# Kernel optimization log

Hardware: AMD Instinct MI355X
Metric: run time of the kernel (lower is better)

## Reference

```python
import jax, jax.numpy as jnp
import numpy as np
from jax import lax

B, L, D = 2, 4096, 2048
H = 16
DK = D // H  # head qk dim == head v dim == 128
CONV = 4
EPS = 1e-5


def _causal_depthwise_conv(x, w):
    # x: [b, l, c], w: [c, K]; torch-style cross-correlation with left padding K-1
    K = w.shape[1]
    xp = jnp.pad(x, ((0, 0), (K - 1, 0), (0, 0)))
    Lx = x.shape[1]
    y = jnp.zeros_like(x)
    for i in range(K):
        y = y + xp[:, i:i + Lx, :] * w[:, i]
    return y


def _l2norm(x):
    return x / jnp.sqrt(jnp.sum(x * x, axis=-1, keepdims=True) + 1e-12)


def _delta_rule(q, k, v, beta):
    # q,k: [b,h,l,dk]; v: [b,h,l,dv]; beta: [b,h,l]
    b, h, l, dk = q.shape
    dv = v.shape[-1]
    qs = jnp.moveaxis(q, 2, 0)
    ks = jnp.moveaxis(k, 2, 0)
    vs = jnp.moveaxis(v, 2, 0)
    bs = jnp.moveaxis(beta, 2, 0)

    def step(S, inp):
        qt, kt, vt, bt = inp  # [b,h,dk],[b,h,dk],[b,h,dv],[b,h]
        kS = jnp.einsum('bhk,bhkv->bhv', kt, S)
        u = bt[..., None] * (vt - kS)
        S = S + kt[..., None] * u[:, :, None, :]
        o = jnp.einsum('bhk,bhkv->bhv', qt, S)
        return S, o

    S0 = jnp.zeros((b, h, dk, dv), dtype=q.dtype)
    _, os = lax.scan(step, S0, (qs, ks, vs, bs))
    return jnp.moveaxis(os, 0, 2)  # [b,h,l,dv]


def setup_inputs() -> dict:
    key = jax.random.key(0)
    ks = jax.random.split(key, 8)
    s = 0.02
    return {
        'hidden_states': jax.random.normal(ks[0], (B, L, D), jnp.float32),
        'w_cattn': jax.random.normal(ks[1], (D, 3 * D), jnp.float32) * s,
        'wq_conv': jax.random.normal(ks[2], (D, CONV), jnp.float32) * 0.3,
        'wk_conv': jax.random.normal(ks[3], (D, CONV), jnp.float32) * 0.3,
        'wv_conv': jax.random.normal(ks[4], (D, CONV), jnp.float32) * 0.3,
        'w_beta': jax.random.normal(ks[5], (D, H), jnp.float32) * s,
        'o_norm_w': jnp.ones((DK,), jnp.float32),
        'w_o': jax.random.normal(ks[6], (D, D), jnp.float32) * s,
    }


def reference(hidden_states, w_cattn, wq_conv, wk_conv, wv_conv, w_beta, o_norm_w, w_o):
    qkv = hidden_states @ w_cattn  # [b,l,3D]
    q, k, v = jnp.split(qkv, 3, axis=-1)
    # short conv + SiLU activation (qk_activation='silu', v conv always SiLU)
    q = jax.nn.silu(_causal_depthwise_conv(q, wq_conv))
    k = jax.nn.silu(_causal_depthwise_conv(k, wk_conv))
    v = jax.nn.silu(_causal_depthwise_conv(v, wv_conv))
    # b l (h d) -> b h l d
    def to_heads(x):
        return jnp.transpose(x.reshape(B, L, H, -1), (0, 2, 1, 3))
    q, k, v = to_heads(q), to_heads(k), to_heads(v)
    # qk_norm = 'l2'
    q = _l2norm(q)
    k = _l2norm(k)
    beta = jax.nn.sigmoid(hidden_states @ w_beta)  # [b,l,h]
    beta = jnp.transpose(beta, (0, 2, 1))  # [b,h,l]
    o = _delta_rule(q, k, v, beta)  # [b,h,l,dv]
    o = jnp.transpose(o, (0, 2, 1, 3))  # [b,l,h,dv]
    # RMSNorm over head_v_dim
    o = o * lax.rsqrt(jnp.mean(o * o, axis=-1, keepdims=True) + EPS) * o_norm_w
    o = o.reshape(B, L, D)
    return o @ w_o
```

## Files before the change

kernel.cpp:

```cpp
#include <hip/hip_runtime.h>
#include <stdint.h>

#define B_   2
#define L_   4096
#define D_   2048
#define H_   16
#define DK_  128
#define ND3  6144
#define BL_  8192

typedef __bf16 bf16x8 __attribute__((ext_vector_type(8)));
typedef float  f32x4  __attribute__((ext_vector_type(4)));

__device__ __forceinline__ float bf2f(ushort u){ return __uint_as_float(((unsigned)u)<<16); }
__device__ __forceinline__ ushort f2bf(float f){
  unsigned u = __float_as_uint(f);
  unsigned r = u + 0x7FFFu + ((u>>16)&1u);
  return (ushort)(r>>16);
}
__device__ __forceinline__ f32x4 mfma16(bf16x8 a, bf16x8 b, f32x4 c){
  return __builtin_amdgcn_mfma_f32_16x16x32_bf16(a, b, c, 0, 0, 0);
}

#define BAR_LGKM() do{ __builtin_amdgcn_sched_barrier(0); \
  asm volatile("s_waitcnt lgkmcnt(0)" ::: "memory"); \
  __builtin_amdgcn_s_barrier(); \
  __builtin_amdgcn_sched_barrier(0);}while(0)
#define BAR_VMALL() do{ __builtin_amdgcn_sched_barrier(0); \
  asm volatile("s_waitcnt vmcnt(0) lgkmcnt(0)" ::: "memory"); \
  __builtin_amdgcn_s_barrier(); \
  __builtin_amdgcn_sched_barrier(0);}while(0)

__global__ __launch_bounds__(256) void k_cast(const float* __restrict__ x, ushort* __restrict__ y, int n4){
  int i = blockIdx.x*blockDim.x + threadIdx.x;
  int stride = gridDim.x*blockDim.x;
  for (; i < n4; i += stride){
    float4 v = ((const float4*)x)[i];
    ushort4 o; o.x=f2bf(v.x); o.y=f2bf(v.y); o.z=f2bf(v.z); o.w=f2bf(v.w);
    ((ushort4*)y)[i] = o;
  }
}

__global__ __launch_bounds__(256) void k_transpose_cast(const float* __restrict__ in, ushort* __restrict__ out,
                                                        int R, int C){
  __shared__ float tile[32][33];
  int c0 = blockIdx.x*32, r0 = blockIdx.y*32;
  int tx = threadIdx.x, ty = threadIdx.y;
  #pragma unroll
  for (int i=0;i<32;i+=8) tile[ty+i][tx] = in[(size_t)(r0+ty+i)*C + (c0+tx)];
  __syncthreads();
  #pragma unroll
  for (int i=0;i<32;i+=8) out[(size_t)(c0+ty+i)*R + (r0+tx)] = f2bf(tile[tx][ty+i]);
}

template<int OUT_BF16>
__global__ __launch_bounds__(512, 1) void k_gemm8(const ushort* __restrict__ A, const ushort* __restrict__ Bt,
                                                  void* __restrict__ Cv, int M, int N, int K){
  __shared__ ushort LDSB[65536];
  char* lds = (char*)LDSB;
  const int tid = threadIdx.x, lane = tid & 63, w = tid >> 6;
  const int wm = w >> 2, wn = w & 3;
  int nwg = gridDim.x*gridDim.y;
  int id  = blockIdx.y*gridDim.x + blockIdx.x;
  int sw  = ((nwg & 7) == 0) ? ((id & 7)*(nwg >> 3) + (id >> 3)) : id;
  const int bx = sw % gridDim.x, by = sw / gridDim.x;
  const int m0 = by*256, n0 = bx*256;
  const int NT = K >> 6;
  const size_t rowb = (size_t)K*2;
  const char* gA = (const char*)A  + (size_t)m0*rowb;
  const char* gB = (const char*)Bt + (size_t)n0*rowb;

  f32x4 acc[8][4];
  #pragma unroll
  for (int i=0;i<8;i++)
    #pragma unroll
    for (int j=0;j<4;j++) acc[i][j] = (f32x4){0.f,0.f,0.f,0.f};

  auto stage = [&](int d2, int which, int T){
    const int isB = which >> 1, h = which & 1;
    const char* g = isB ? gB : gA;
    char* halfbase = lds + d2*65536 + isB*32768 + h*16384;
    #pragma unroll
    for (int uu=0; uu<2; ++uu){
      int u = tid + uu*512;
      int band = u >> 7, kk = (u >> 6) & 1, lr = u & 15, lk = (u >> 4) & 3;
      const char* src = g + (size_t)(h*128 + band*16 + lr)*rowb + (size_t)T*128 + kk*64 + lk*16;
      __builtin_amdgcn_global_load_lds(
        (const __attribute__((address_space(1))) void*)src,
        (__attribute__((address_space(3))) void*)(halfbase + u*16), 16, 0, 0);
    }
  };

  stage(0, 0, 0); stage(0, 1, 0); stage(0, 2, 0); stage(0, 3, 0);
  {
    int t1 = (1 < NT) ? 1 : 0;
    stage(1, 0, t1); stage(1, 3, t1);
  }
  asm volatile("s_waitcnt vmcnt(4)" ::: "memory");
  __builtin_amdgcn_s_barrier();

  for (int t = 0; t < NT; ++t){
    const int d = t & 1;
    const char* bufb = lds + d*65536;
    const int tn1 = (t+1 < NT) ? t+1 : NT-1;
    const int tn2 = (t+2 < NT) ? t+2 : NT-1;

    bf16x8 afr[4][2];
    bf16x8 b0r[2][2], b1r[2][2];

    #pragma unroll
    for (int il=0; il<4; ++il)
      #pragma unroll
      for (int kk=0; kk<2; ++kk)
        afr[il][kk] = *(const bf16x8*)(bufb + ((wm*4+il)*2+kk)*1024 + lane*16);
    #pragma unroll
    for (int jl=0; jl<2; ++jl)
      #pragma unroll
      for (int kk=0; kk<2; ++kk)
        b0r[jl][kk] = *(const bf16x8*)(bufb + 32768 + ((wn*2+jl)*2+kk)*1024 + lane*16);
    stage(d^1, 1, tn1);
    __builtin_amdgcn_s_barrier();
    __builtin_amdgcn_s_setprio(1);
    #pragma unroll
    for (int kk=0; kk<2; ++kk)
      #pragma unroll
      for (int il=0; il<4; ++il)
        #pragma unroll
        for (int jl=0; jl<2; ++jl)
          acc[il][jl] = mfma16(afr[il][kk], b0r[jl][kk], acc[il][jl]);
    __builtin_amdgcn_s_setprio(0);
    __builtin_amdgcn_s_barrier();

    #pragma unroll
    for (int jl=0; jl<2; ++jl)
      #pragma unroll
      for (int kk=0; kk<2; ++kk)
        b1r[jl][kk] = *(const bf16x8*)(bufb + 32768 + 16384 + ((wn*2+jl)*2+kk)*1024 + lane*16);
    stage(d^1, 2, tn1);
    __builtin_amdgcn_s_barrier();
    __builtin_amdgcn_s_setprio(1);
    #pragma unroll
    for (int kk=0; kk<2; ++kk)
      #pragma unroll
      for (int il=0; il<4; ++il)
        #pragma unroll
        for (int jl=0; jl<2; ++jl)
          acc[il][2+jl] = mfma16(afr[il][kk], b1r[jl][kk], acc[il][2+jl]);
    __builtin_amdgcn_s_setprio(0);
    __builtin_amdgcn_s_barrier();

    #pragma unroll
    for (int il=0; il<4; ++il)
      #pragma unroll
      for (int kk=0; kk<2; ++kk)
        afr[il][kk] = *(const bf16x8*)(bufb + 16384 + ((wm*4+il)*2+kk)*1024 + lane*16);
    stage(d, 0, tn2);
    __builtin_amdgcn_s_barrier();
    __builtin_amdgcn_s_setprio(1);
    #pragma unroll
    for (int kk=0; kk<2; ++kk)
      #pragma unroll
      for (int il=0; il<4; ++il)
        #pragma unroll
        for (int jl=0; jl<2; ++jl)
          acc[4+il][2+jl] = mfma16(afr[il][kk], b1r[jl][kk], acc[4+il][2+jl]);
    __builtin_amdgcn_s_setprio(0);
    __builtin_amdgcn_s_barrier();

    stage(d, 3, tn2);
    __builtin_amdgcn_s_barrier();
    __builtin_amdgcn_s_setprio(1);
    #pragma unroll
    for (int kk=0; kk<2; ++kk)
      #pragma unroll
      for (int il=0; il<4; ++il)
        #pragma unroll
        for (int jl=0; jl<2; ++jl)
          acc[4+il][jl] = mfma16(afr[il][kk], b0r[jl][kk], acc[4+il][jl]);
    __builtin_amdgcn_s_setprio(0);
    asm volatile("s_waitcnt vmcnt(4)" ::: "memory");
    __builtin_amdgcn_s_barrier();
  }
  asm volatile("s_waitcnt vmcnt(0) lgkmcnt(0)" ::: "memory");

  #pragma unroll
  for (int fi=0; fi<8; ++fi){
    int row0 = m0 + (fi>>2)*128 + wm*64 + (fi&3)*16 + (lane>>4)*4;
    #pragma unroll
    for (int fj=0; fj<4; ++fj){
      int col = n0 + (fj>>1)*128 + wn*32 + (fj&1)*16 + (lane&15);
      #pragma unroll
      for (int r=0; r<4; ++r){
        float v = acc[fi][fj][r];
        if (OUT_BF16) ((ushort*)Cv)[(size_t)(row0+r)*N + col] = f2bf(v);
        else          ((float*) Cv)[(size_t)(row0+r)*N + col] = v;
      }
    }
  }
}

__global__ __launch_bounds__(256) void k_wbt(const float* __restrict__ wb, ushort* __restrict__ wbT){
  int d = blockIdx.x*256 + threadIdx.x;
  #pragma unroll
  for (int h=0;h<16;h++) wbT[(size_t)h*2048 + d] = f2bf(wb[(size_t)d*16 + h]);
}

__global__ __launch_bounds__(64) void k_beta2(const ushort* __restrict__ A16, const ushort* __restrict__ wbT,
                                              float* __restrict__ beta){
  const int rt = blockIdx.x;
  const int lane = threadIdx.x;
  const int lr = lane & 15, lk8 = (lane>>4)*8;
  const int r0 = rt*16;
  f32x4 acc0 = (f32x4){0.f,0.f,0.f,0.f};
  f32x4 acc1 = (f32x4){0.f,0.f,0.f,0.f};
  for (int k0=0; k0<2048; k0+=64){
    bf16x8 a0 = *(const bf16x8*)&A16[(size_t)(r0+lr)*2048 + k0 + lk8];
    bf16x8 b0 = *(const bf16x8*)&wbT[(size_t)lr*2048 + k0 + lk8];
    bf16x8 a1 = *(const bf16x8*)&A16[(size_t)(r0+lr)*2048 + k0 + 32 + lk8];
    bf16x8 b1 = *(const bf16x8*)&wbT[(size_t)lr*2048 + k0 + 32 + lk8];
    acc0 = mfma16(a0, b0, acc0);
    acc1 = mfma16(a1, b1, acc1);
  }
  const int h = lane & 15;
  const int rbase = r0 + (lane>>4)*4;
  #pragma unroll
  for (int r=0;r<4;r++){
    int row = rbase + r;
    int b = row >> 12, l = row & 4095;
    float sg = 1.f/(1.f + __expf(-(acc0[r] + acc1[r])));
    beta[((size_t)(b*H_ + h))*L_ + l] = sg;
  }
}

__global__ __launch_bounds__(256) void k_conv2(const ushort* __restrict__ qkv,
      const float* __restrict__ wq, const float* __restrict__ wk, const float* __restrict__ wv,
      ushort* __restrict__ QH, ushort* __restrict__ KH, ushort* __restrict__ VH){
  const int seg = blockIdx.x, part = blockIdx.y, b = blockIdx.z;
  const int t = threadIdx.x;
  const int ch = t*8;
  const int h = t >> 4, d0 = (t & 15)*8;
  const float* wc = (part==0) ? wq : (part==1) ? wk : wv;
  ushort* outs = ((part==0) ? QH : (part==1) ? KH : VH)
                 + ((size_t)(b*H_ + h)*L_)*DK_ + d0;
  const ushort* inp = qkv + ((size_t)b*L_)*ND3 + part*D_ + ch;

  float wgt[4][8];
  #pragma unroll
  for (int j=0;j<8;j++){
    float4 w4 = *(const float4*)&wc[(ch + j)*4];
    wgt[0][j]=w4.x; wgt[1][j]=w4.y; wgt[2][j]=w4.z; wgt[3][j]=w4.w;
  }

  const int l0 = seg*32;
  float x0[8], x1[8], x2[8];
  {
    float* dsts[3] = {x0, x1, x2};
    #pragma unroll
    for (int i=0;i<3;i++){
      int l = l0 - 3 + i;
      float* d = dsts[i];
      if (l >= 0){
        const ushort* p = inp + (size_t)l*ND3;
        ushort4 a = *(const ushort4*)p, c = *(const ushort4*)(p+4);
        d[0]=bf2f(a.x); d[1]=bf2f(a.y); d[2]=bf2f(a.z); d[3]=bf2f(a.w);
        d[4]=bf2f(c.x); d[5]=bf2f(c.y); d[6]=bf2f(c.z); d[7]=bf2f(c.w);
      } else {
        #pragma unroll
        for (int j=0;j<8;j++) d[j] = 0.f;
      }
    }
  }

  for (int i=0;i<32;i++){
    const int l = l0 + i;
    float cur[8];
    {
      const ushort* p = inp + (size_t)l*ND3;
      ushort4 a = *(const ushort4*)p, c = *(const ushort4*)(p+4);
      cur[0]=bf2f(a.x); cur[1]=bf2f(a.y); cur[2]=bf2f(a.z); cur[3]=bf2f(a.w);
      cur[4]=bf2f(c.x); cur[5]=bf2f(c.y); cur[6]=bf2f(c.z); cur[7]=bf2f(c.w);
    }
    float y[8]; float ss = 0.f;
    #pragma unroll
    for (int j=0;j<8;j++){
      float yy = x0[j]*wgt[0][j] + x1[j]*wgt[1][j] + x2[j]*wgt[2][j] + cur[j]*wgt[3][j];
      yy = yy / (1.f + __expf(-yy));
      y[j] = yy; ss += yy*yy;
    }
    if (part < 2){
      #pragma unroll
      for (int m=1;m<16;m<<=1) ss += __shfl_xor(ss, m, 64);
      float sc = rsqrtf(ss + 1e-12f);
      #pragma unroll
      for (int j=0;j<8;j++) y[j] *= sc;
    }
    ushort4 o0, o1;
    o0.x=f2bf(y[0]); o0.y=f2bf(y[1]); o0.z=f2bf(y[2]); o0.w=f2bf(y[3]);
    o1.x=f2bf(y[4]); o1.y=f2bf(y[5]); o1.z=f2bf(y[6]); o1.w=f2bf(y[7]);
    ushort* op = outs + (size_t)l*DK_;
    *(ushort4*)op = o0; *(ushort4*)(op+4) = o1;
    #pragma unroll
    for (int j=0;j<8;j++){ x0[j]=x1[j]; x1[j]=x2[j]; x2[j]=cur[j]; }
  }
}

__global__ __launch_bounds__(64) void k_prep(const ushort* __restrict__ QH, const ushort* __restrict__ KH,
      const float* __restrict__ BETA, ushort* __restrict__ TB, ushort* __restrict__ MM,
      ushort* __restrict__ KT){
  const int bid = blockIdx.x, bh = bid>>6, c = bid&63;
  const int lane = threadIdx.x;
  __shared__ ushort Ks[64][136];
  __shared__ __align__(16) char QA[17408];
  __shared__ float bs[64];
  ushort (*Qs)[136] = (ushort (*)[136])QA;
  float  (*As)[64]  = (float  (*)[64])QA;

  const ushort* kg = KH + ((size_t)bh*L_ + c*64)*DK_;
  const ushort* qg = QH + ((size_t)bh*L_ + c*64)*DK_;
  {
    const uint4* ks4 = (const uint4*)(kg + (size_t)lane*DK_);
    const uint4* qs4 = (const uint4*)(qg + (size_t)lane*DK_);
    uint4* kd = (uint4*)&Ks[lane][0];
    uint4* qd = (uint4*)&Qs[lane][0];
    #pragma unroll
    for (int i=0;i<16;i++){ kd[i] = ks4[i]; qd[i] = qs4[i]; }
    bs[lane] = BETA[(size_t)bh*L_ + c*64 + lane];
  }
  __syncthreads();
  const int lr = lane&15, lk = lane>>4;

  f32x4 gac[4][4];
  #pragma unroll
  for (int i=0;i<4;i++)
    #pragma unroll
    for (int j=0;j<4;j++) gac[i][j] = (f32x4){0.f,0.f,0.f,0.f};
  #pragma unroll
  for (int kk=0;kk<4;kk++){
    bf16x8 fr[4];
    #pragma unroll
    for (int i=0;i<4;i++) fr[i] = *(const bf16x8*)&Ks[i*16+lr][kk*32 + lk*8];
    #pragma unroll
    for (int mi=0;mi<4;mi++)
      #pragma unroll
      for (int ni=0;ni<4;ni++)
        gac[mi][ni] = mfma16(fr[mi], fr[ni], gac[mi][ni]);
  }
  {
    f32x4 mac[4][4];
    #pragma unroll
    for (int i=0;i<4;i++)
      #pragma unroll
      for (int j=0;j<4;j++) mac[i][j] = (f32x4){0.f,0.f,0.f,0.f};
    #pragma unroll
    for (int kk=0;kk<4;kk++){
      bf16x8 frq[4], frk[4];
      #pragma unroll
      for (int i=0;i<4;i++){
        frq[i] = *(const bf16x8*)&Qs[i*16+lr][kk*32 + lk*8];
        frk[i] = *(const bf16x8*)&Ks[i*16+lr][kk*32 + lk*8];
      }
      #pragma unroll
      for (int mi=0;mi<4;mi++)
        #pragma unroll
        for (int ni=0;ni<4;ni++)
          mac[mi][ni] = mfma16(frq[mi], frk[ni], mac[mi][ni]);
    }
    #pragma unroll
    for (int mi=0;mi<4;mi++)
      #pragma unroll
      for (int ni=0;ni<4;ni++)
        #pragma unroll
        for (int r=0;r<4;r++){
          int t = mi*16 + lk*4 + r, s = ni*16 + lr;
          float v = (s <= t) ? mac[mi][ni][r] : 0.f;
          MM[(size_t)bid*4096 + t*64 + s] = f2bf(v);
        }
  }
  __syncthreads();

  #pragma unroll
  for (int mi=0;mi<4;mi++)
    #pragma unroll
    for (int ni=0;ni<4;ni++)
      #pragma unroll
      for (int r=0;r<4;r++){
        int t = mi*16 + lk*4 + r, s = ni*16 + lr;
        As[t][s] = (s < t) ? (bs[t] * gac[mi][ni][r]) : 0.f;
      }
  __syncthreads();

  float rT[64];
  #pragma unroll
  for (int t=0;t<64;t++){
    float arow = As[t][lane];
    float a = (t==lane) ? 1.f : 0.f;
    #pragma unroll
    for (int s=0;s<t;s++){
      float cc = __int_as_float(__builtin_amdgcn_readlane(__float_as_int(arow), s));
      a -= cc * rT[s];
    }
    rT[t] = a;
  }
  {
    float bc = bs[lane];
    #pragma unroll
    for (int t=0;t<64;t++)
      TB[(size_t)bid*4096 + t*64 + lane] = f2bf(rT[t] * bc);
  }
  for (int d2=0; d2<64; d2++){
    unsigned uu = *(const unsigned*)&Ks[lane][2*d2];
    KT[(size_t)bid*8192 + (size_t)(2*d2)*64 + lane]   = (ushort)(uu & 0xffffu);
    KT[(size_t)bid*8192 + (size_t)(2*d2+1)*64 + lane] = (ushort)(uu >> 16);
  }
}

template<int LRB, int GRB, int NB, int XM>
__device__ __forceinline__ void stage_swz(const ushort* __restrict__ g, ushort* l,
                                          int colOff, int w, int lane){
  for (int idx = w; idx < NB/1024; idx += 4){
    int off = idx*1024 + lane*16;
    int row = off / LRB;
    int inner = off & (LRB-1);
    int src = row*GRB + colOff + (inner ^ ((row&XM)<<4));
    __builtin_amdgcn_global_load_lds(
      (const __attribute__((address_space(1))) void*)((const char*)g + src),
      (__attribute__((address_space(3))) void*)((char*)l + idx*1024), 16, 0, 0);
  }
}

__global__ __launch_bounds__(256) void k_chunkrec(const ushort* __restrict__ QH, const ushort* __restrict__ KH,
      const ushort* __restrict__ VH, const ushort* __restrict__ TB, const ushort* __restrict__ MM,
      const ushort* __restrict__ KT, ushort* __restrict__ OH){
  const int p = blockIdx.x;
  const int xg = p & 7, s = p >> 3;
  const int bh = xg + (s >> 3)*8;
  const int vo = s & 7;
  const int tid = threadIdx.x, lane = tid&63, w = tid>>6;
  const int lr = lane&15, lk = lane>>4;
  const int tw = w*16;
  const int dw = w*32;

  __shared__ ushort SM[71680];
  ushort* Stl = SM + 67584;
  ushort* Ztl = SM + 69632;
  ushort* Utl = SM + 70656;

  const ushort* kbase  = KH + ((size_t)bh*L_)*DK_;
  const ushort* qbase  = QH + ((size_t)bh*L_)*DK_;
  const ushort* vbase  = VH + ((size_t)bh*L_)*DK_;
  const ushort* tbase  = TB + ((size_t)bh*64)*4096;
  const ushort* mbase  = MM + ((size_t)bh*64)*4096;
  const ushort* ktbase = KT + ((size_t)bh*64)*8192;
  ushort* obase = OH + ((size_t)bh*L_)*DK_ + vo*16;

  auto stageall = [&](ushort* buf, int c){
    stage_swz<256,256,16384,7>(kbase  + (size_t)c*8192, buf,         0,     w, lane);
    stage_swz<256,256,16384,7>(qbase  + (size_t)c*8192, buf + 8192,  0,     w, lane);
    stage_swz<128,128,16384,7>(ktbase + (size_t)c*8192, buf + 16384, 0,     w, lane);
    stage_swz<128,128, 8192,7>(tbase  + (size_t)c*4096, buf + 24576, 0,     w, lane);
    stage_swz<128,128, 8192,7>(mbase  + (size_t)c*4096, buf + 28672, 0,     w, lane);
    stage_swz< 32,256, 2048,0>(vbase  + (size_t)c*8192, buf + 32768, vo*32, w, lane);
  };

  f32x4 Stf[2];
  Stf[0] = (f32x4){0.f,0.f,0.f,0.f};
  Stf[1] = (f32x4){0.f,0.f,0.f,0.f};

  stageall(SM, 0);
  BAR_VMALL();

  for (int c=0; c<64; ++c){
    ushort* buf  = SM + (c&1)*33792;
    ushort* nbuf = SM + ((c+1)&1)*33792;
    const ushort* Kc  = buf;
    const ushort* Qc  = buf + 8192;
    const ushort* Ktc = buf + 16384;
    const ushort* Tbc = buf + 24576;
    const ushort* Mc  = buf + 28672;
    const ushort* Vc  = buf + 32768;

    if (c+1 < 64) stageall(nbuf, c+1);

    #pragma unroll
    for (int nd=0;nd<2;nd++)
      #pragma unroll
      for (int r=0;r<4;r++){
        int j = lk*4 + r;
        int d = dw + nd*16 + lr;
        Stl[j*128 + (d ^ ((j&7)<<3))] = f2bf(Stf[nd][r]);
      }
    BAR_LGKM();

    f32x4 xac = (f32x4){0.f,0.f,0.f,0.f};
    #pragma unroll
    for (int kk=0;kk<4;kk++){
      int e = kk*32 + lk*8;
      int ta = tw + lr;
      bf16x8 ak  = *(const bf16x8*)&Kc[ta*128 + (e ^ ((ta&7)<<3))];
      bf16x8 bst = *(const bf16x8*)&Stl[lr*128 + (e ^ ((lr&7)<<3))];
      xac = mfma16(ak, bst, xac);
    }
    #pragma unroll
    for (int r=0;r<4;r++){
      int t = tw + lk*4 + r;
      int j = lr;
      float v = bf2f(Vc[t*16 + j]);
      Ztl[j*64 + (t ^ ((j&7)<<3))] = f2bf(v - xac[r]);
    }
    BAR_LGKM();

    f32x4 uac = (f32x4){0.f,0.f,0.f,0.f};
    #pragma unroll
    for (int kk=0;kk<2;kk++){
      int e = kk*32 + lk*8;
      int ta = tw + lr;
      bf16x8 at = *(const bf16x8*)&Tbc[ta*64 + (e ^ ((ta&7)<<3))];
      bf16x8 bz = *(const bf16x8*)&Ztl[lr*64 + (e ^ ((lr&7)<<3))];
      uac = mfma16(at, bz, uac);
    }
    #pragma unroll
    for (int r=0;r<4;r++){
      int t = tw + lk*4 + r;
      int j = lr;
      Utl[j*64 + (t ^ ((j&7)<<3))] = f2bf(uac[r]);
    }
    BAR_LGKM();

    f32x4 oac = (f32x4){0.f,0.f,0.f,0.f};
    #pragma unroll
    for (int kk=0;kk<4;kk++){
      int e = kk*32 + lk*8;
      int ta = tw + lr;
      bf16x8 aq  = *(const bf16x8*)&Qc[ta*128 + (e ^ ((ta&7)<<3))];
      bf16x8 bst = *(const bf16x8*)&Stl[lr*128 + (e ^ ((lr&7)<<3))];
      oac = mfma16(aq, bst, oac);
    }
    #pragma unroll
    for (int kk=0;kk<2;kk++){
      int e = kk*32 + lk*8;
      int ta = tw + lr;
      bf16x8 am = *(const bf16x8*)&Mc[ta*64 + (e ^ ((ta&7)<<3))];
      bf16x8 bu = *(const bf16x8*)&Utl[lr*64 + (e ^ ((lr&7)<<3))];
      oac = mfma16(am, bu, oac);
    }
    #pragma unroll
    for (int r=0;r<4;r++){
      int t = tw + lk*4 + r;
      int j = lr;
      obase[(size_t)(c*64 + t)*DK_ + j] = f2bf(oac[r]);
    }

    #pragma unroll
    for (int kk=0;kk<2;kk++){
      int e = kk*32 + lk*8;
      bf16x8 au = *(const bf16x8*)&Utl[lr*64 + (e ^ ((lr&7)<<3))];
      #pragma unroll
      for (int nd=0;nd<2;nd++){
        int d = dw + nd*16 + lr;
        bf16x8 bk = *(const bf16x8*)&Ktc[d*64 + (e ^ ((d&7)<<3))];
        Stf[nd] = mfma16(au, bk, Stf[nd]);
      }
    }
    BAR_VMALL();
  }
}

__global__ __launch_bounds__(256) void k_norm(const ushort* __restrict__ OH, const float* __restrict__ gw,
                                              ushort* __restrict__ O2){
  const int blk = blockIdx.x;
  const int b = blk >> 12, l = blk & 4095;
  const int t = threadIdx.x;
  const int h = t >> 4, d0 = (t & 15) * 8;
  const ushort* ip = OH + ((size_t)(b*H_ + h)*L_ + l)*DK_ + d0;
  ushort4 a = *(const ushort4*)ip, c = *(const ushort4*)(ip+4);
  float x[8];
  x[0]=bf2f(a.x); x[1]=bf2f(a.y); x[2]=bf2f(a.z); x[3]=bf2f(a.w);
  x[4]=bf2f(c.x); x[5]=bf2f(c.y); x[6]=bf2f(c.z); x[7]=bf2f(c.w);
  float ss = 0.f;
  #pragma unroll
  for (int j=0;j<8;j++) ss += x[j]*x[j];
  #pragma unroll
  for (int m=1;m<16;m<<=1) ss += __shfl_xor(ss, m, 64);
  float sc = rsqrtf(ss * (1.f/128.f) + 1e-5f);
  ushort* opp = O2 + (size_t)blk*D_ + h*DK_ + d0;
  ushort4 o0, o1;
  o0.x=f2bf(x[0]*sc*gw[d0+0]); o0.y=f2bf(x[1]*sc*gw[d0+1]);
  o0.z=f2bf(x[2]*sc*gw[d0+2]); o0.w=f2bf(x[3]*sc*gw[d0+3]);
  o1.x=f2bf(x[4]*sc*gw[d0+4]); o1.y=f2bf(x[5]*sc*gw[d0+5]);
  o1.z=f2bf(x[6]*sc*gw[d0+6]); o1.w=f2bf(x[7]*sc*gw[d0+7]);
  *(ushort4*)opp = o0; *(ushort4*)(opp+4) = o1;
}

extern "C" void kernel_launch(void* const* d_in, const int* in_sizes, int n_in,
                              void* d_out, int out_size, void* d_ws, size_t ws_size,
                              hipStream_t stream) {
  (void)in_sizes; (void)n_in; (void)out_size; (void)ws_size;
  const float* hidden  = (const float*)d_in[0];
  const float* w_cattn = (const float*)d_in[1];
  const float* wq_conv = (const float*)d_in[2];
  const float* wk_conv = (const float*)d_in[3];
  const float* wv_conv = (const float*)d_in[4];
  const float* w_beta  = (const float*)d_in[5];
  const float* o_nw    = (const float*)d_in[6];
  const float* w_o     = (const float*)d_in[7];
  float* out = (float*)d_out;

  char* W = (char*)d_ws;
  ushort* A16   = (ushort*)(W);
  ushort* WcatT = (ushort*)(W + 33554432u);
  ushort* WoT   = (ushort*)(W + 33554432u);
  float*  BETA  = (float*) (W + 41943040u);
  ushort* WBT   = (ushort*)(W + 42467328u);
  ushort* QKV   = (ushort*)(W + 58720256u);
  ushort* TB    = (ushort*)(W + 58720256u);
  ushort* MM    = (ushort*)(W + 75497472u);
  ushort* KT    = (ushort*)(W + 92274688u);
  ushort* O2    = (ushort*)(W + 125829120u);
  ushort* QH    = (ushort*)(W + 159383552u);
  ushort* KH    = (ushort*)(W + 192937984u);
  ushort* VH    = (ushort*)(W + 226492416u);
  ushort* OH = A16;

  k_cast<<<4096, 256, 0, stream>>>(hidden, A16, (BL_*D_)/4);
  k_transpose_cast<<<dim3(ND3/32, D_/32), dim3(32,8), 0, stream>>>(w_cattn, WcatT, D_, ND3);
  k_gemm8<1><<<dim3(ND3/256, BL_/256), 512, 0, stream>>>(A16, WcatT, QKV, BL_, ND3, D_);
  k_transpose_cast<<<dim3(D_/32, D_/32), dim3(32,8), 0, stream>>>(w_o, WoT, D_, D_);
  k_wbt<<<8, 256, 0, stream>>>(w_beta, WBT);
  k_beta2<<<512, 64, 0, stream>>>(A16, WBT, BETA);
  k_conv2<<<dim3(128, 3, 2), 256, 0, stream>>>(QKV, wq_conv, wk_conv, wv_conv, QH, KH, VH);
  k_prep<<<2048, 64, 0, stream>>>(QH, KH, BETA, TB, MM, KT);
  k_chunkrec<<<256, 256, 0, stream>>>(QH, KH, VH, TB, MM, KT, OH);
  k_norm<<<BL_, 256, 0, stream>>>(OH, o_nw, O2);
  k_gemm8<0><<<dim3(D_/256, BL_/256), 512, 0, stream>>>(O2, WoT, out, BL_, D_, D_);
}
```

Baseline: 574.5 us.

## Compute QK mask and K transpose inside chunk recurrence instead of prep

Moves the masked Q·K^T chunk matrix and the K transpose out of the prep kernel and into the chunk recurrence. There they are computed from the already-staged K and Q tiles in LDS. This removes writing and re-reading the MM and KT buffers through global memory and shrinks the per-chunk staging footprint. The cost is redundant recomputation across the eight value-slice blocks per head and more work inside the serial chunk loop.

```diff
diff --git a/kernel.cpp b/kernel.cpp
--- a/kernel.cpp
+++ b/kernel.cpp
@@ -304,26 +304,20 @@
   }
 }
 
-__global__ __launch_bounds__(64) void k_prep(const ushort* __restrict__ QH, const ushort* __restrict__ KH,
-      const float* __restrict__ BETA, ushort* __restrict__ TB, ushort* __restrict__ MM,
-      ushort* __restrict__ KT){
+__global__ __launch_bounds__(64) void k_prep(const ushort* __restrict__ KH,
+      const float* __restrict__ BETA, ushort* __restrict__ TB){
   const int bid = blockIdx.x, bh = bid>>6, c = bid&63;
   const int lane = threadIdx.x;
   __shared__ ushort Ks[64][136];
-  __shared__ __align__(16) char QA[17408];
+  __shared__ float As[64][64];
   __shared__ float bs[64];
-  ushort (*Qs)[136] = (ushort (*)[136])QA;
-  float  (*As)[64]  = (float  (*)[64])QA;
 
   const ushort* kg = KH + ((size_t)bh*L_ + c*64)*DK_;
-  const ushort* qg = QH + ((size_t)bh*L_ + c*64)*DK_;
   {
     const uint4* ks4 = (const uint4*)(kg + (size_t)lane*DK_);
-    const uint4* qs4 = (const uint4*)(qg + (size_t)lane*DK_);
     uint4* kd = (uint4*)&Ks[lane][0];
-    uint4* qd = (uint4*)&Qs[lane][0];
-    #pragma unroll
-    for (int i=0;i<16;i++){ kd[i] = ks4[i]; qd[i] = qs4[i]; }
+    #pragma unroll
+    for (int i=0;i<16;i++) kd[i] = ks4[i];
     bs[lane] = BETA[(size_t)bh*L_ + c*64 + lane];
   }
   __syncthreads();
@@ -345,39 +339,6 @@
       for (int ni=0;ni<4;ni++)
         gac[mi][ni] = mfma16(fr[mi], fr[ni], gac[mi][ni]);
   }
-  {
-    f32x4 mac[4][4];
-    #pragma unroll
-    for (int i=0;i<4;i++)
-      #pragma unroll
-      for (int j=0;j<4;j++) mac[i][j] = (f32x4){0.f,0.f,0.f,0.f};
-    #pragma unroll
-    for (int kk=0;kk<4;kk++){
-      bf16x8 frq[4], frk[4];
-      #pragma unroll
-      for (int i=0;i<4;i++){
-        frq[i] = *(const bf16x8*)&Qs[i*16+lr][kk*32 + lk*8];
-        frk[i] = *(const bf16x8*)&Ks[i*16+lr][kk*32 + lk*8];
-      }
-      #pragma unroll
-      for (int mi=0;mi<4;mi++)
-        #pragma unroll
-        for (int ni=0;ni<4;ni++)
-          mac[mi][ni] = mfma16(frq[mi], frk[ni], mac[mi][ni]);
-    }
-    #pragma unroll
-    for (int mi=0;mi<4;mi++)
-      #pragma unroll
-      for (int ni=0;ni<4;ni++)
-        #pragma unroll
-        for (int r=0;r<4;r++){
-          int t = mi*16 + lk*4 + r, s = ni*16 + lr;
-          float v = (s <= t) ? mac[mi][ni][r] : 0.f;
-          MM[(size_t)bid*4096 + t*64 + s] = f2bf(v);
-        }
-  }
-  __syncthreads();
-
   #pragma unroll
   for (int mi=0;mi<4;mi++)
     #pragma unroll
@@ -406,11 +367,6 @@
     #pragma unroll
     for (int t=0;t<64;t++)
       TB[(size_t)bid*4096 + t*64 + lane] = f2bf(rT[t] * bc);
-  }
-  for (int d2=0; d2<64; d2++){
-    unsigned uu = *(const unsigned*)&Ks[lane][2*d2];
-    KT[(size_t)bid*8192 + (size_t)(2*d2)*64 + lane]   = (ushort)(uu & 0xffffu);
-    KT[(size_t)bid*8192 + (size_t)(2*d2+1)*64 + lane] = (ushort)(uu >> 16);
   }
 }
 
@@ -429,8 +385,7 @@
 }
 
 __global__ __launch_bounds__(256) void k_chunkrec(const ushort* __restrict__ QH, const ushort* __restrict__ KH,
-      const ushort* __restrict__ VH, const ushort* __restrict__ TB, const ushort* __restrict__ MM,
-      const ushort* __restrict__ KT, ushort* __restrict__ OH){
+      const ushort* __restrict__ VH, const ushort* __restrict__ TB, ushort* __restrict__ OH){
   const int p = blockIdx.x;
   const int xg = p & 7, s = p >> 3;
   const int bh = xg + (s >> 3)*8;
@@ -440,26 +395,24 @@
   const int tw = w*16;
   const int dw = w*32;
 
-  __shared__ ushort SM[71680];
-  ushort* Stl = SM + 67584;
-  ushort* Ztl = SM + 69632;
-  ushort* Utl = SM + 70656;
+  __shared__ ushort SM[59392];
+  ushort* Stl = SM + 43008;
+  ushort* Ztl = SM + 45056;
+  ushort* Utl = SM + 46080;
+  ushort* Mc  = SM + 47104;
+  ushort* Ktc = SM + 51200;
 
   const ushort* kbase  = KH + ((size_t)bh*L_)*DK_;
   const ushort* qbase  = QH + ((size_t)bh*L_)*DK_;
   const ushort* vbase  = VH + ((size_t)bh*L_)*DK_;
   const ushort* tbase  = TB + ((size_t)bh*64)*4096;
-  const ushort* mbase  = MM + ((size_t)bh*64)*4096;
-  const ushort* ktbase = KT + ((size_t)bh*64)*8192;
   ushort* obase = OH + ((size_t)bh*L_)*DK_ + vo*16;
 
   auto stageall = [&](ushort* buf, int c){
-    stage_swz<256,256,16384,7>(kbase  + (size_t)c*8192, buf,         0,     w, lane);
-    stage_swz<256,256,16384,7>(qbase  + (size_t)c*8192, buf + 8192,  0,     w, lane);
-    stage_swz<128,128,16384,7>(ktbase + (size_t)c*8192, buf + 16384, 0,     w, lane);
-    stage_swz<128,128, 8192,7>(tbase  + (size_t)c*4096, buf + 24576, 0,     w, lane);
-    stage_swz<128,128, 8192,7>(mbase  + (size_t)c*4096, buf + 28672, 0,     w, lane);
-    stage_swz< 32,256, 2048,0>(vbase  + (size_t)c*8192, buf + 32768, vo*32, w, lane);
+    stage_swz<256,256,16384,7>(kbase + (size_t)c*8192, buf,         0,     w, lane);
+    stage_swz<256,256,16384,7>(qbase + (size_t)c*8192, buf + 8192,  0,     w, lane);
+    stage_swz<128,128, 8192,7>(tbase + (size_t)c*4096, buf + 16384, 0,     w, lane);
+    stage_swz< 32,256, 2048,0>(vbase + (size_t)c*8192, buf + 20480, vo*32, w, lane);
   };
 
   f32x4 Stf[2];
@@ -470,14 +423,12 @@
   BAR_VMALL();
 
   for (int c=0; c<64; ++c){
-    ushort* buf  = SM + (c&1)*33792;
-    ushort* nbuf = SM + ((c+1)&1)*33792;
+    ushort* buf  = SM + (c&1)*21504;
+    ushort* nbuf = SM + ((c+1)&1)*21504;
     const ushort* Kc  = buf;
     const ushort* Qc  = buf + 8192;
-    const ushort* Ktc = buf + 16384;
-    const ushort* Tbc = buf + 24576;
-    const ushort* Mc  = buf + 28672;
-    const ushort* Vc  = buf + 32768;
+    const ushort* Tbc = buf + 16384;
+    const ushort* Vc  = buf + 20480;
 
     if (c+1 < 64) stageall(nbuf, c+1);
 
@@ -489,6 +440,41 @@
         int d = dw + nd*16 + lr;
         Stl[j*128 + (d ^ ((j&7)<<3))] = f2bf(Stf[nd][r]);
       }
+    {
+      const int tt = tid & 63, dp0 = tid >> 6;
+      #pragma unroll
+      for (int i=0;i<16;i++){
+        int dp = dp0 + 4*i;
+        unsigned kk2 = *(const unsigned*)&Kc[tt*128 + ((2*dp) ^ ((tt&7)<<3))];
+        Ktc[(2*dp)*64   + (tt ^ (((2*dp)&7)<<3))]   = (ushort)(kk2 & 0xffffu);
+        Ktc[(2*dp+1)*64 + (tt ^ (((2*dp+1)&7)<<3))] = (ushort)(kk2 >> 16);
+      }
+    }
+    {
+      f32x4 mac[4];
+      #pragma unroll
+      for (int ni=0;ni<4;ni++) mac[ni] = (f32x4){0.f,0.f,0.f,0.f};
+      #pragma unroll
+      for (int kk=0;kk<4;kk++){
+        int e = kk*32 + lk*8;
+        int ta = tw + lr;
+        bf16x8 aq = *(const bf16x8*)&Qc[ta*128 + (e ^ ((ta&7)<<3))];
+        #pragma unroll
+        for (int ni=0;ni<4;ni++){
+          int sr = ni*16 + lr;
+          bf16x8 bk = *(const bf16x8*)&Kc[sr*128 + (e ^ ((sr&7)<<3))];
+          mac[ni] = mfma16(aq, bk, mac[ni]);
+        }
+      }
+      #pragma unroll
+      for (int ni=0;ni<4;ni++)
+        #pragma unroll
+        for (int r=0;r<4;r++){
+          int t = tw + lk*4 + r, sc2 = ni*16 + lr;
+          float v = (sc2 <= t) ? mac[ni][r] : 0.f;
+          Mc[t*64 + (sc2 ^ ((t&7)<<3))] = f2bf(v);
+        }
+    }
     BAR_LGKM();
 
     f32x4 xac = (f32x4){0.f,0.f,0.f,0.f};
@@ -613,8 +599,6 @@
   ushort* WBT   = (ushort*)(W + 42467328u);
   ushort* QKV   = (ushort*)(W + 58720256u);
   ushort* TB    = (ushort*)(W + 58720256u);
-  ushort* MM    = (ushort*)(W + 75497472u);
-  ushort* KT    = (ushort*)(W + 92274688u);
   ushort* O2    = (ushort*)(W + 125829120u);
   ushort* QH    = (ushort*)(W + 159383552u);
   ushort* KH    = (ushort*)(W + 192937984u);
@@ -628,8 +612,8 @@
   k_wbt<<<8, 256, 0, stream>>>(w_beta, WBT);
   k_beta2<<<512, 64, 0, stream>>>(A16, WBT, BETA);
   k_conv2<<<dim3(128, 3, 2), 256, 0, stream>>>(QKV, wq_conv, wk_conv, wv_conv, QH, KH, VH);
-  k_prep<<<2048, 64, 0, stream>>>(QH, KH, BETA, TB, MM, KT);
-  k_chunkrec<<<256, 256, 0, stream>>>(QH, KH, VH, TB, MM, KT, OH);
+  k_prep<<<2048, 64, 0, stream>>>(KH, BETA, TB);
+  k_chunkrec<<<256, 256, 0, stream>>>(QH, KH, VH, TB, OH);
   k_norm<<<BL_, 256, 0, stream>>>(OH, o_nw, O2);
   k_gemm8<0><<<dim3(D_/256, BL_/256), 512, 0, stream>>>(O2, WoT, out, BL_, D_, D_);
 }
```

New measurement: 610.3 us. 1.06x slower.
